# Kernel tuning notes

Measured on AMD Instinct MI355X. Metric: run time of the kernel, lower is better.

## Reference

```python
import jax, jax.numpy as jnp
import numpy as np

N = 8192        # n_nodes
F = 256         # n_features
RES_H = 512     # n_res_hidden
REP_H = 256     # n_rep_hidden
EMB = 128       # embed_dim
E = 262144      # n_edges
GAMMA = 0.1


def setup_inputs() -> dict:
    key = jax.random.key(0)
    ks = jax.random.split(key, 20)
    w = lambda k, shape, s=0.05: (jax.random.normal(k, shape, jnp.float32) * s)
    return {
        "x": jax.random.normal(ks[0], (N, F), jnp.float32),
        "edge_index": jax.random.randint(ks[1], (2, E), 0, N),
        # res_model: Linear(N,RES_H)+ReLU, Linear(RES_H,F)+ReLU
        "res_W1": w(ks[2], (N, RES_H)), "res_b1": jnp.zeros((RES_H,), jnp.float32),
        "res_W2": w(ks[3], (RES_H, F)), "res_b2": jnp.zeros((F,), jnp.float32),
        "fc_W1": w(ks[4], (F, REP_H)), "fc_b1": jnp.zeros((REP_H,), jnp.float32),
        "fc_W2": w(ks[5], (REP_H, REP_H)), "fc_b2": jnp.zeros((REP_H,), jnp.float32),
        # rep_gcn: GCNConv(F,REP_H,norm=False), GCNConv(REP_H,REP_H), GCNConv(REP_H,EMB)
        "g_W0": w(ks[6], (F, REP_H)), "g_b0": jnp.zeros((REP_H,), jnp.float32),
        "g_W1": w(ks[7], (REP_H, REP_H)), "g_b1": jnp.zeros((REP_H,), jnp.float32),
        "g_W2": w(ks[8], (REP_H, EMB)), "g_b2": jnp.zeros((EMB,), jnp.float32),
        # dec_fc: Linear(EMB,REP_H)+ReLU, Linear(REP_H,F)+ReLU
        "dec_W1": w(ks[9], (EMB, REP_H)), "dec_b1": jnp.zeros((REP_H,), jnp.float32),
        "dec_W2": w(ks[10], (REP_H, F)), "dec_b2": jnp.zeros((F,), jnp.float32),
    }


def _gcn(h, src, dst, W, b, normalize):
    """PyG GCNConv: transform then aggregate src->dst; sym-norm with self loops if normalize."""
    h = h @ W
    if normalize:
        ones = jnp.ones(src.shape[0], h.dtype)
        deg = jax.ops.segment_sum(ones, dst, num_segments=N) + 1.0  # +1 self loop
        dinv = jax.lax.rsqrt(deg)
        coef = dinv[src] * dinv[dst]
        agg = jax.ops.segment_sum(h[src] * coef[:, None], dst, num_segments=N)
        agg = agg + h * (dinv * dinv)[:, None]  # self-loop message
    else:
        agg = jax.ops.segment_sum(h[src], dst, num_segments=N)
    return agg + b


def _fwd(x, edge_index, res_W1, res_b1, res_W2, res_b2, fc_W1, fc_b1, fc_W2, fc_b2,
         g_W0, g_b0, g_W1, g_b1, g_W2, g_b2, dec_W1, dec_b1, dec_W2, dec_b2):
    relu = jax.nn.relu
    src, dst = edge_index[0], edge_index[1]
    # dense adjacency (to_dense_adj accumulates edge weights = 1)
    A = jnp.zeros((N, N), x.dtype).at[src, dst].add(1.0)
    # residual model over adjacency rows
    R = relu(relu(A @ res_W1 + res_b1) @ res_W2 + res_b2)  # [N, F]
    # GCN layer 0 (normalize=False)
    H = relu(_gcn(x, src, dst, g_W0, g_b0, False))
    # layer 1
    R_l = relu(R @ fc_W1 + fc_b1)
    H = relu(_gcn(H * jnp.exp(-GAMMA * R_l), src, dst, g_W1, g_b1, True))
    # layer 2
    R_l = relu(R_l @ fc_W2 + fc_b2)
    H = relu(_gcn(H * jnp.exp(-GAMMA * R_l), src, dst, g_W2, g_b2, True))  # [N, EMB]
    X_hat = relu(relu(H @ dec_W1 + dec_b1) @ dec_W2 + dec_b2)  # [N, F]
    A_hat = H @ H.T  # [N, N]
    return X_hat, A_hat, R


def reference(x, edge_index, res_W1, res_b1, res_W2, res_b2, fc_W1, fc_b1, fc_W2, fc_b2,
              g_W0, g_b0, g_W1, g_b1, g_W2, g_b2, dec_W1, dec_b1, dec_W2, dec_b2):
    return _fwd(x, edge_index, res_W1, res_b1, res_W2, res_b2, fc_W1, fc_b1, fc_W2, fc_b2,
                g_W0, g_b0, g_W1, g_b1, g_W2, g_b2, dec_W1, dec_b1, dec_W2, dec_b2)
```

## Files before the change

### kernel.cpp

```cpp
#include <hip/hip_runtime.h>
#include <cstddef>
#include <cstdint>

#define NN   8192
#define FF   256
#define RESH 512
#define REPH 256
#define EMBD 128
#define EE   262144
#define GAMMA_ 0.1f

typedef __attribute__((ext_vector_type(8))) short bf16x8;
typedef __attribute__((ext_vector_type(4))) float f32x4;

__device__ inline void f2hilo(float x, short& h, short& l) {
  unsigned u = __float_as_uint(x);
  unsigned r = u + 0x7FFFu + ((u >> 16) & 1u);
  h = (short)(r >> 16);
  float hf = __uint_as_float(r & 0xFFFF0000u);
  float lf = x - hf;
  unsigned u2 = __float_as_uint(lf);
  unsigned r2 = u2 + 0x7FFFu + ((u2 >> 16) & 1u);
  l = (short)(r2 >> 16);
}


__global__ void count_kernel(const int* __restrict__ ei, int* __restrict__ cnt_src,
                             int* __restrict__ cnt_dst) {
  int e = blockIdx.x * blockDim.x + threadIdx.x;
  if (e < EE) {
    atomicAdd(&cnt_src[ei[e]], 1);
    atomicAdd(&cnt_dst[ei[EE + e]], 1);
  }
}

__global__ void scan_kernel(const int* __restrict__ cnt_src, const int* __restrict__ cnt_dst,
                            int* __restrict__ off_src, int* __restrict__ off_dst) {
  const int* cnt = blockIdx.x ? cnt_dst : cnt_src;
  int* off = blockIdx.x ? off_dst : off_src;
  __shared__ int sm[1024];
  int carry = 0;
  for (int ch = 0; ch < NN / 1024; ++ch) {
    int idx = ch * 1024 + threadIdx.x;
    int v = cnt[idx];
    int x = v;
    sm[threadIdx.x] = x;
    __syncthreads();
    for (int ofs = 1; ofs < 1024; ofs <<= 1) {
      int y = (threadIdx.x >= ofs) ? sm[threadIdx.x - ofs] : 0;
      __syncthreads();
      x += y;
      sm[threadIdx.x] = x;
      __syncthreads();
    }
    off[idx] = x - v + carry;
    carry += sm[1023];
    __syncthreads();
  }
  if (threadIdx.x == 0) off[NN] = carry;
}

__global__ void fill_kernel(const int* __restrict__ ei, const int* __restrict__ off_src,
                            const int* __restrict__ off_dst, int* __restrict__ cur_src,
                            int* __restrict__ cur_dst, int* __restrict__ adj_src,
                            int* __restrict__ adj_dst) {
  int e = blockIdx.x * blockDim.x + threadIdx.x;
  if (e < EE) {
    int s = ei[e], d = ei[EE + e];
    int ps = atomicAdd(&cur_src[s], 1);
    adj_src[off_src[s] + ps] = d;
    int pd = atomicAdd(&cur_dst[d], 1);
    adj_dst[off_dst[d] + pd] = s;
  }
}

__global__ void dinv_kernel(const int* __restrict__ cnt_dst, float* __restrict__ dinv) {
  int n = blockIdx.x * blockDim.x + threadIdx.x;
  if (n < NN) dinv[n] = rsqrtf((float)cnt_dst[n] + 1.0f);
}

__global__ __launch_bounds__(256) void s1_kernel(const float* __restrict__ W1,
    const float* __restrict__ b1, const int* __restrict__ off_src,
    const int* __restrict__ adj_src, float* __restrict__ S1) {
  int i = blockIdx.x, t = threadIdx.x;
  int beg = off_src[i], end = off_src[i + 1];
  float a0 = 0.f, a1 = 0.f;
#pragma unroll 4
  for (int k = beg; k < end; ++k) {
    int d = adj_src[k];
    const float* row = W1 + (size_t)d * RESH;
    a0 += row[t];
    a1 += row[t + 256];
  }
  S1[(size_t)i * RESH + t]       = fmaxf(a0 + b1[t], 0.f);
  S1[(size_t)i * RESH + t + 256] = fmaxf(a1 + b1[t + 256], 0.f);
}

__global__ __launch_bounds__(256) void agg0_kernel(const float* __restrict__ h,
    const float* __restrict__ b, const int* __restrict__ off_dst,
    const int* __restrict__ adj_dst, float* __restrict__ out) {
  int d = blockIdx.x, t = threadIdx.x;
  int beg = off_dst[d], end = off_dst[d + 1];
  float acc = 0.f;
#pragma unroll 4
  for (int k = beg; k < end; ++k) {
    int s = adj_dst[k];
    acc += h[(size_t)s * REPH + t];
  }
  out[(size_t)d * REPH + t] = fmaxf(acc + b[t], 0.f);
}

__global__ void aggn_kernel(const float* __restrict__ h, const float* __restrict__ b,
    const float* __restrict__ dinv, const int* __restrict__ off_dst,
    const int* __restrict__ adj_dst, float* __restrict__ out, int C) {
  int d = blockIdx.x, t = threadIdx.x;
  int beg = off_dst[d], end = off_dst[d + 1];
  float acc = 0.f;
#pragma unroll 4
  for (int k = beg; k < end; ++k) {
    int s = adj_dst[k];
    acc += h[(size_t)s * C + t] * dinv[s];
  }
  float dd = dinv[d];
  float v = acc * dd + h[(size_t)d * C + t] * dd * dd + b[t];
  out[(size_t)d * C + t] = fmaxf(v, 0.f);
}

struct WDesc { const float* src; short* h; short* l; int K; int N; };
struct WTab { WDesc d[8]; };

__global__ void prep_w(WTab tab) {
  WDesc d = tab.d[blockIdx.y];
  int total = d.K * d.N;
  for (int i = blockIdx.x * 256 + threadIdx.x; i < total; i += 128 * 256) {
    int n = i / d.K, k = i - n * d.K;
    float x = d.src[(size_t)k * d.N + n];
    short hh, ll;
    f2hilo(x, hh, ll);
    d.h[i] = hh;
    d.l[i] = ll;
  }
}

__global__ void conv_h(const float* __restrict__ Hf, short* __restrict__ Hh,
                       short* __restrict__ Hl) {
  int i = blockIdx.x * 256 + threadIdx.x;
  float x = Hf[i];
  short hh, ll;
  f2hilo(x, hh, ll);
  Hh[i] = hh;
  Hl[i] = ll;
}

__global__ __launch_bounds__(256) void gemmW(const float* __restrict__ A,
    const float* __restrict__ Rm, const short* __restrict__ Wh,
    const short* __restrict__ Wl, const float* __restrict__ bias,
    float* __restrict__ C, int K, int Nc, int doRelu) {
  const int w = threadIdx.x >> 6, l = threadIdx.x & 63;
  const int lr = l & 15, lk = l >> 4;
  const int m0 = blockIdx.y * 64 + w * 16;
  const int n0 = blockIdx.x * 128;
  f32x4 acc[8] = {};
  const int nks = K >> 5;
  for (int ks = 0; ks < nks; ++ks) {
    const int k0 = (ks << 5) + (lk << 3);
    const float* ap = A + (size_t)(m0 + lr) * K + k0;
    float av[8];
    *(f32x4*)(av + 0) = *(const f32x4*)(ap + 0);
    *(f32x4*)(av + 4) = *(const f32x4*)(ap + 4);
    if (Rm) {
      const float* rp = Rm + (size_t)(m0 + lr) * K + k0;
      float rv[8];
      *(f32x4*)(rv + 0) = *(const f32x4*)(rp + 0);
      *(f32x4*)(rv + 4) = *(const f32x4*)(rp + 4);
#pragma unroll
      for (int j = 0; j < 8; ++j) av[j] *= expf(-GAMMA_ * rv[j]);
    }
    bf16x8 ah, al;
#pragma unroll
    for (int j = 0; j < 8; ++j) {
      short hh, ll;
      f2hilo(av[j], hh, ll);
      ah[j] = hh;
      al[j] = ll;
    }
#pragma unroll
    for (int cb = 0; cb < 8; ++cb) {
      size_t boff = (size_t)(n0 + (cb << 4) + lr) * K + k0;
      bf16x8 bh = *(const bf16x8*)(Wh + boff);
      bf16x8 bl = *(const bf16x8*)(Wl + boff);
      acc[cb] = __builtin_amdgcn_mfma_f32_16x16x32_bf16(ah, bh, acc[cb], 0, 0, 0);
      acc[cb] = __builtin_amdgcn_mfma_f32_16x16x32_bf16(al, bh, acc[cb], 0, 0, 0);
      acc[cb] = __builtin_amdgcn_mfma_f32_16x16x32_bf16(ah, bl, acc[cb], 0, 0, 0);
    }
  }
#pragma unroll
  for (int cb = 0; cb < 8; ++cb) {
    int col = n0 + (cb << 4) + lr;
    float bv = bias ? bias[col] : 0.f;
#pragma unroll
    for (int r = 0; r < 4; ++r) {
      int row = m0 + (lk << 2) + r;
      float v = acc[cb][r] + bv;
      if (doRelu) v = fmaxf(v, 0.f);
      C[(size_t)row * Nc + col] = v;
    }
  }
}

__global__ __launch_bounds__(256) void ahat_mfma(const short* __restrict__ Hh,
    const short* __restrict__ Hl, float* __restrict__ C) {
  const int w = threadIdx.x >> 6, l = threadIdx.x & 63;
  const int lr = l & 15, lk = l >> 4;
  const int bi = blockIdx.y * 128 + w * 32;
  const int bj = blockIdx.x * 128;
  f32x4 acc[2][8] = {};
#pragma unroll
  for (int ks = 0; ks < 4; ++ks) {
    const int k0 = (ks << 5) + (lk << 3);
    bf16x8 ah[2], al[2];
#pragma unroll
    for (int rb = 0; rb < 2; ++rb) {
      size_t off = (size_t)(bi + (rb << 4) + lr) * EMBD + k0;
      ah[rb] = *(const bf16x8*)(Hh + off);
      al[rb] = *(const bf16x8*)(Hl + off);
    }
#pragma unroll
    for (int cb = 0; cb < 8; ++cb) {
      size_t off = (size_t)(bj + (cb << 4) + lr) * EMBD + k0;
      bf16x8 bh = *(const bf16x8*)(Hh + off);
      bf16x8 bl = *(const bf16x8*)(Hl + off);
#pragma unroll
      for (int rb = 0; rb < 2; ++rb) {
        acc[rb][cb] = __builtin_amdgcn_mfma_f32_16x16x32_bf16(ah[rb], bh, acc[rb][cb], 0, 0, 0);
        acc[rb][cb] = __builtin_amdgcn_mfma_f32_16x16x32_bf16(al[rb], bh, acc[rb][cb], 0, 0, 0);
        acc[rb][cb] = __builtin_amdgcn_mfma_f32_16x16x32_bf16(ah[rb], bl, acc[rb][cb], 0, 0, 0);
      }
    }
  }
#pragma unroll
  for (int rb = 0; rb < 2; ++rb)
#pragma unroll
    for (int cb = 0; cb < 8; ++cb) {
      int row = bi + (rb << 4) + (lk << 2);
      int col = bj + (cb << 4) + lr;
#pragma unroll
      for (int r = 0; r < 4; ++r)
        C[(size_t)(row + r) * NN + col] = acc[rb][cb][r];
    }
}


extern "C" void kernel_launch(void* const* d_in, const int* in_sizes, int n_in,
                              void* d_out, int out_size, void* d_ws, size_t ws_size,
                              hipStream_t stream) {
  const float* x      = (const float*)d_in[0];
  const int*   ei     = (const int*)d_in[1];
  const float* res_W1 = (const float*)d_in[2];
  const float* res_b1 = (const float*)d_in[3];
  const float* res_W2 = (const float*)d_in[4];
  const float* res_b2 = (const float*)d_in[5];
  const float* fc_W1  = (const float*)d_in[6];
  const float* fc_b1  = (const float*)d_in[7];
  const float* fc_W2  = (const float*)d_in[8];
  const float* fc_b2  = (const float*)d_in[9];
  const float* g_W0   = (const float*)d_in[10];
  const float* g_b0   = (const float*)d_in[11];
  const float* g_W1   = (const float*)d_in[12];
  const float* g_b1   = (const float*)d_in[13];
  const float* g_W2   = (const float*)d_in[14];
  const float* g_b2   = (const float*)d_in[15];
  const float* dec_W1 = (const float*)d_in[16];
  const float* dec_b1 = (const float*)d_in[17];
  const float* dec_W2 = (const float*)d_in[18];
  const float* dec_b2 = (const float*)d_in[19];

  float* out   = (float*)d_out;
  float* X_hat = out;
  float* A_hat = out + (size_t)NN * FF;
  float* R     = A_hat + (size_t)NN * NN;

  char* ws = (char*)d_ws;
  size_t o = 0;
  auto alloc = [&](size_t bytes) -> void* {
    void* p = ws + o;
    o += (bytes + 1023) & ~(size_t)1023;
    return p;
  };
  int* cnt_src = (int*)alloc(NN * 4);
  int* cnt_dst = (int*)alloc(NN * 4);
  int* cur_src = (int*)alloc(NN * 4);
  int* cur_dst = (int*)alloc(NN * 4);
  int* off_src = (int*)alloc((NN + 1) * 4);
  int* off_dst = (int*)alloc((NN + 1) * 4);
  int* adj_src = (int*)alloc((size_t)EE * 4);
  int* adj_dst = (int*)alloc((size_t)EE * 4);
  float* dinv  = (float*)alloc(NN * 4);
  float* S1    = (float*)alloc((size_t)NN * RESH * 4);
  float* B1    = (float*)alloc((size_t)NN * REPH * 4);
  float* B2    = (float*)alloc((size_t)NN * REPH * 4);
  float* B3    = (float*)alloc((size_t)NN * REPH * 4);
  float* B4    = (float*)alloc((size_t)NN * REPH * 4);
  short* Wt_h  = (short*)alloc(524288 * 2);
  short* Wt_l  = (short*)alloc(524288 * 2);
  short* Hh    = (short*)alloc((size_t)NN * EMBD * 2);
  short* Hl    = (short*)alloc((size_t)NN * EMBD * 2);

  const int o_resW2 = 0;
  const int o_fcW1  = 131072;
  const int o_fcW2  = 196608;
  const int o_gW0   = 262144;
  const int o_gW1   = 327680;
  const int o_gW2   = 393216;
  const int o_decW1 = 425984;
  const int o_decW2 = 458752;

  hipMemsetAsync(cnt_src, 0, (size_t)NN * 4 * 4, stream);

  count_kernel<<<EE / 256, 256, 0, stream>>>(ei, cnt_src, cnt_dst);
  scan_kernel<<<2, 1024, 0, stream>>>(cnt_src, cnt_dst, off_src, off_dst);
  fill_kernel<<<EE / 256, 256, 0, stream>>>(ei, off_src, off_dst, cur_src, cur_dst,
                                            adj_src, adj_dst);
  dinv_kernel<<<NN / 256, 256, 0, stream>>>(cnt_dst, dinv);

  WTab tab;
  tab.d[0] = {res_W2, Wt_h + o_resW2, Wt_l + o_resW2, RESH, FF};
  tab.d[1] = {fc_W1,  Wt_h + o_fcW1,  Wt_l + o_fcW1,  FF,   REPH};
  tab.d[2] = {fc_W2,  Wt_h + o_fcW2,  Wt_l + o_fcW2,  REPH, REPH};
  tab.d[3] = {g_W0,   Wt_h + o_gW0,   Wt_l + o_gW0,   FF,   REPH};
  tab.d[4] = {g_W1,   Wt_h + o_gW1,   Wt_l + o_gW1,   REPH, REPH};
  tab.d[5] = {g_W2,   Wt_h + o_gW2,   Wt_l + o_gW2,   REPH, EMBD};
  tab.d[6] = {dec_W1, Wt_h + o_decW1, Wt_l + o_decW1, EMBD, REPH};
  tab.d[7] = {dec_W2, Wt_h + o_decW2, Wt_l + o_decW2, REPH, FF};
  prep_w<<<dim3(128, 8), 256, 0, stream>>>(tab);

  s1_kernel<<<NN, 256, 0, stream>>>(res_W1, res_b1, off_src, adj_src, S1);
  gemmW<<<dim3(FF / 128, NN / 64), 256, 0, stream>>>(S1, nullptr, Wt_h + o_resW2,
      Wt_l + o_resW2, res_b2, R, RESH, FF, 1);
  gemmW<<<dim3(REPH / 128, NN / 64), 256, 0, stream>>>(x, nullptr, Wt_h + o_gW0,
      Wt_l + o_gW0, nullptr, B1, FF, REPH, 0);
  agg0_kernel<<<NN, REPH, 0, stream>>>(B1, g_b0, off_dst, adj_dst, B2);
  gemmW<<<dim3(REPH / 128, NN / 64), 256, 0, stream>>>(R, nullptr, Wt_h + o_fcW1,
      Wt_l + o_fcW1, fc_b1, B3, FF, REPH, 1);
  gemmW<<<dim3(REPH / 128, NN / 64), 256, 0, stream>>>(B2, B3, Wt_h + o_gW1,
      Wt_l + o_gW1, nullptr, B1, REPH, REPH, 0);
  aggn_kernel<<<NN, REPH, 0, stream>>>(B1, g_b1, dinv, off_dst, adj_dst, B2, REPH);
  gemmW<<<dim3(REPH / 128, NN / 64), 256, 0, stream>>>(B3, nullptr, Wt_h + o_fcW2,
      Wt_l + o_fcW2, fc_b2, B4, REPH, REPH, 1);
  gemmW<<<dim3(EMBD / 128, NN / 64), 256, 0, stream>>>(B2, B4, Wt_h + o_gW2,
      Wt_l + o_gW2, nullptr, B3, REPH, EMBD, 0);
  aggn_kernel<<<NN, EMBD, 0, stream>>>(B3, g_b2, dinv, off_dst, adj_dst, B1, EMBD);
  conv_h<<<(NN * EMBD) / 256, 256, 0, stream>>>(B1, Hh, Hl);
  gemmW<<<dim3(REPH / 128, NN / 64), 256, 0, stream>>>(B1, nullptr, Wt_h + o_decW1,
      Wt_l + o_decW1, dec_b1, B2, EMBD, REPH, 1);
  gemmW<<<dim3(FF / 128, NN / 64), 256, 0, stream>>>(B2, nullptr, Wt_h + o_decW2,
      Wt_l + o_decW2, dec_b2, X_hat, REPH, FF, 1);
  ahat_mfma<<<dim3(NN / 128, NN / 128), 256, 0, stream>>>(Hh, Hl, A_hat);
}
```

Baseline: 881.3 us.

## Pre-split activations into bf16 hi/lo in producers and exploit A_hat symmetry

Result: faster. 800.2 us (-9.2%).

```diff
diff --git a/kernel.cpp b/kernel.cpp
--- a/kernel.cpp
+++ b/kernel.cpp
@@ -1,6 +1,7 @@
 #include <hip/hip_runtime.h>
 #include <cstddef>
 #include <cstdint>
+#include <math.h>
 
 #define NN   8192
 #define FF   256
@@ -12,6 +13,7 @@
 
 typedef __attribute__((ext_vector_type(8))) short bf16x8;
 typedef __attribute__((ext_vector_type(4))) float f32x4;
+typedef __attribute__((ext_vector_type(4))) short s16x4;
 
 __device__ inline void f2hilo(float x, short& h, short& l) {
   unsigned u = __float_as_uint(x);
@@ -81,7 +83,7 @@
 
 __global__ __launch_bounds__(256) void s1_kernel(const float* __restrict__ W1,
     const float* __restrict__ b1, const int* __restrict__ off_src,
-    const int* __restrict__ adj_src, float* __restrict__ S1) {
+    const int* __restrict__ adj_src, short* __restrict__ S1h, short* __restrict__ S1l) {
   int i = blockIdx.x, t = threadIdx.x;
   int beg = off_src[i], end = off_src[i + 1];
   float a0 = 0.f, a1 = 0.f;
@@ -92,13 +94,21 @@
     a0 += row[t];
     a1 += row[t + 256];
   }
-  S1[(size_t)i * RESH + t]       = fmaxf(a0 + b1[t], 0.f);
-  S1[(size_t)i * RESH + t + 256] = fmaxf(a1 + b1[t + 256], 0.f);
-}
-
-__global__ __launch_bounds__(256) void agg0_kernel(const float* __restrict__ h,
-    const float* __restrict__ b, const int* __restrict__ off_dst,
-    const int* __restrict__ adj_dst, float* __restrict__ out) {
+  float v0 = fmaxf(a0 + b1[t], 0.f);
+  float v1 = fmaxf(a1 + b1[t + 256], 0.f);
+  short hh, ll;
+  f2hilo(v0, hh, ll);
+  S1h[(size_t)i * RESH + t] = hh;
+  S1l[(size_t)i * RESH + t] = ll;
+  f2hilo(v1, hh, ll);
+  S1h[(size_t)i * RESH + t + 256] = hh;
+  S1l[(size_t)i * RESH + t + 256] = ll;
+}
+
+__global__ __launch_bounds__(256) void agg0_fused(const float* __restrict__ h,
+    const float* __restrict__ b, const float* __restrict__ mod,
+    const int* __restrict__ off_dst, const int* __restrict__ adj_dst,
+    short* __restrict__ oh, short* __restrict__ ol) {
   int d = blockIdx.x, t = threadIdx.x;
   int beg = off_dst[d], end = off_dst[d + 1];
   float acc = 0.f;
@@ -107,12 +117,18 @@
     int s = adj_dst[k];
     acc += h[(size_t)s * REPH + t];
   }
-  out[(size_t)d * REPH + t] = fmaxf(acc + b[t], 0.f);
-}
-
-__global__ void aggn_kernel(const float* __restrict__ h, const float* __restrict__ b,
-    const float* __restrict__ dinv, const int* __restrict__ off_dst,
-    const int* __restrict__ adj_dst, float* __restrict__ out, int C) {
+  size_t o = (size_t)d * REPH + t;
+  float v = fmaxf(acc + b[t], 0.f) * expf(-GAMMA_ * mod[o]);
+  short hh, ll;
+  f2hilo(v, hh, ll);
+  oh[o] = hh;
+  ol[o] = ll;
+}
+
+__global__ void aggn_fused(const float* __restrict__ h, const float* __restrict__ b,
+    const float* __restrict__ dinv, const float* __restrict__ mod,
+    const int* __restrict__ off_dst, const int* __restrict__ adj_dst,
+    short* __restrict__ oh, short* __restrict__ ol, int C) {
   int d = blockIdx.x, t = threadIdx.x;
   int beg = off_dst[d], end = off_dst[d + 1];
   float acc = 0.f;
@@ -122,8 +138,13 @@
     acc += h[(size_t)s * C + t] * dinv[s];
   }
   float dd = dinv[d];
-  float v = acc * dd + h[(size_t)d * C + t] * dd * dd + b[t];
-  out[(size_t)d * C + t] = fmaxf(v, 0.f);
+  size_t o = (size_t)d * C + t;
+  float v = fmaxf(acc * dd + h[o] * dd * dd + b[t], 0.f);
+  if (mod) v *= expf(-GAMMA_ * mod[o]);
+  short hh, ll;
+  f2hilo(v, hh, ll);
+  oh[o] = hh;
+  ol[o] = ll;
 }
 
 struct WDesc { const float* src; short* h; short* l; int K; int N; };
@@ -142,50 +163,41 @@
   }
 }
 
-__global__ void conv_h(const float* __restrict__ Hf, short* __restrict__ Hh,
-                       short* __restrict__ Hl) {
-  int i = blockIdx.x * 256 + threadIdx.x;
-  float x = Hf[i];
-  short hh, ll;
-  f2hilo(x, hh, ll);
-  Hh[i] = hh;
-  Hl[i] = ll;
-}
-
-__global__ __launch_bounds__(256) void gemmW(const float* __restrict__ A,
-    const float* __restrict__ Rm, const short* __restrict__ Wh,
-    const short* __restrict__ Wl, const float* __restrict__ bias,
-    float* __restrict__ C, int K, int Nc, int doRelu) {
+__global__ void conv_split(const float* __restrict__ in, short* __restrict__ oh,
+                           short* __restrict__ ol) {
+  int i = (blockIdx.x * 256 + threadIdx.x) * 4;
+  f32x4 v = *(const f32x4*)(in + i);
+  s16x4 vh, vl;
+#pragma unroll
+  for (int j = 0; j < 4; ++j) {
+    short hh, ll;
+    f2hilo(v[j], hh, ll);
+    vh[j] = hh;
+    vl[j] = ll;
+  }
+  *(s16x4*)(oh + i) = vh;
+  *(s16x4*)(ol + i) = vl;
+}
+
+template<int CB>
+__global__ __launch_bounds__(256) void gemmS(const short* __restrict__ Ah,
+    const short* __restrict__ Al, const short* __restrict__ Wh,
+    const short* __restrict__ Wl, const float* __restrict__ bias, int doRelu,
+    float* __restrict__ outF, short* __restrict__ outH, short* __restrict__ outL,
+    int K, int Nc) {
   const int w = threadIdx.x >> 6, l = threadIdx.x & 63;
   const int lr = l & 15, lk = l >> 4;
   const int m0 = blockIdx.y * 64 + w * 16;
-  const int n0 = blockIdx.x * 128;
-  f32x4 acc[8] = {};
+  const int n0 = blockIdx.x * (CB * 16);
+  f32x4 acc[CB] = {};
   const int nks = K >> 5;
   for (int ks = 0; ks < nks; ++ks) {
     const int k0 = (ks << 5) + (lk << 3);
-    const float* ap = A + (size_t)(m0 + lr) * K + k0;
-    float av[8];
-    *(f32x4*)(av + 0) = *(const f32x4*)(ap + 0);
-    *(f32x4*)(av + 4) = *(const f32x4*)(ap + 4);
-    if (Rm) {
-      const float* rp = Rm + (size_t)(m0 + lr) * K + k0;
-      float rv[8];
-      *(f32x4*)(rv + 0) = *(const f32x4*)(rp + 0);
-      *(f32x4*)(rv + 4) = *(const f32x4*)(rp + 4);
-#pragma unroll
-      for (int j = 0; j < 8; ++j) av[j] *= expf(-GAMMA_ * rv[j]);
-    }
-    bf16x8 ah, al;
-#pragma unroll
-    for (int j = 0; j < 8; ++j) {
-      short hh, ll;
-      f2hilo(av[j], hh, ll);
-      ah[j] = hh;
-      al[j] = ll;
-    }
-#pragma unroll
-    for (int cb = 0; cb < 8; ++cb) {
+    size_t aoff = (size_t)(m0 + lr) * K + k0;
+    bf16x8 ah = *(const bf16x8*)(Ah + aoff);
+    bf16x8 al = *(const bf16x8*)(Al + aoff);
+#pragma unroll
+    for (int cb = 0; cb < CB; ++cb) {
       size_t boff = (size_t)(n0 + (cb << 4) + lr) * K + k0;
       bf16x8 bh = *(const bf16x8*)(Wh + boff);
       bf16x8 bl = *(const bf16x8*)(Wl + boff);
@@ -195,7 +207,7 @@
     }
   }
 #pragma unroll
-  for (int cb = 0; cb < 8; ++cb) {
+  for (int cb = 0; cb < CB; ++cb) {
     int col = n0 + (cb << 4) + lr;
     float bv = bias ? bias[col] : 0.f;
 #pragma unroll
@@ -203,17 +215,31 @@
       int row = m0 + (lk << 2) + r;
       float v = acc[cb][r] + bv;
       if (doRelu) v = fmaxf(v, 0.f);
-      C[(size_t)row * Nc + col] = v;
-    }
-  }
-}
-
-__global__ __launch_bounds__(256) void ahat_mfma(const short* __restrict__ Hh,
+      size_t off = (size_t)row * Nc + col;
+      if (outF) outF[off] = v;
+      if (outH) {
+        short hh, ll;
+        f2hilo(v, hh, ll);
+        outH[off] = hh;
+        outL[off] = ll;
+      }
+    }
+  }
+}
+
+__global__ __launch_bounds__(256) void ahat_sym(const short* __restrict__ Hh,
     const short* __restrict__ Hl, float* __restrict__ C) {
+  __shared__ float sm[128][129];
+  int z = blockIdx.x;
+  int b = (int)((sqrtf(8.f * (float)z + 1.f) - 1.f) * 0.5f);
+  while ((b + 1) * (b + 2) / 2 <= z) ++b;
+  while (b * (b + 1) / 2 > z) --b;
+  int a = z - b * (b + 1) / 2;
+  const int bi = a * 128, bj = b * 128;
+  const bool mirror = (a != b);
   const int w = threadIdx.x >> 6, l = threadIdx.x & 63;
   const int lr = l & 15, lk = l >> 4;
-  const int bi = blockIdx.y * 128 + w * 32;
-  const int bj = blockIdx.x * 128;
+  const int ri = w * 32;
   f32x4 acc[2][8] = {};
 #pragma unroll
   for (int ks = 0; ks < 4; ++ks) {
@@ -221,7 +247,7 @@
     bf16x8 ah[2], al[2];
 #pragma unroll
     for (int rb = 0; rb < 2; ++rb) {
-      size_t off = (size_t)(bi + (rb << 4) + lr) * EMBD + k0;
+      size_t off = (size_t)(bi + ri + (rb << 4) + lr) * EMBD + k0;
       ah[rb] = *(const bf16x8*)(Hh + off);
       al[rb] = *(const bf16x8*)(Hl + off);
     }
@@ -242,12 +268,22 @@
   for (int rb = 0; rb < 2; ++rb)
 #pragma unroll
     for (int cb = 0; cb < 8; ++cb) {
-      int row = bi + (rb << 4) + (lk << 2);
-      int col = bj + (cb << 4) + lr;
-#pragma unroll
-      for (int r = 0; r < 4; ++r)
-        C[(size_t)(row + r) * NN + col] = acc[rb][cb][r];
-    }
+      int r0 = ri + (rb << 4) + (lk << 2);
+      int c0 = (cb << 4) + lr;
+#pragma unroll
+      for (int r = 0; r < 4; ++r) {
+        float v = acc[rb][cb][r];
+        C[(size_t)(bi + r0 + r) * NN + bj + c0] = v;
+        if (mirror) sm[r0 + r][c0] = v;
+      }
+    }
+  if (mirror) {
+    __syncthreads();
+    for (int idx = threadIdx.x; idx < 128 * 128; idx += 256) {
+      int jr = idx >> 7, c = idx & 127;
+      C[(size_t)(bj + jr) * NN + bi + c] = sm[c][jr];
+    }
+  }
 }
 
 
@@ -296,15 +332,27 @@
   int* adj_src = (int*)alloc((size_t)EE * 4);
   int* adj_dst = (int*)alloc((size_t)EE * 4);
   float* dinv  = (float*)alloc(NN * 4);
-  float* S1    = (float*)alloc((size_t)NN * RESH * 4);
-  float* B1    = (float*)alloc((size_t)NN * REPH * 4);
-  float* B2    = (float*)alloc((size_t)NN * REPH * 4);
-  float* B3    = (float*)alloc((size_t)NN * REPH * 4);
-  float* B4    = (float*)alloc((size_t)NN * REPH * 4);
   short* Wt_h  = (short*)alloc(524288 * 2);
   short* Wt_l  = (short*)alloc(524288 * 2);
-  short* Hh    = (short*)alloc((size_t)NN * EMBD * 2);
-  short* Hl    = (short*)alloc((size_t)NN * EMBD * 2);
+  const size_t SLAB = (size_t)8 * 1024 * 1024;
+  char* slabA = (char*)alloc(SLAB);
+  char* slabB = (char*)alloc(SLAB);
+  char* slabC = (char*)alloc(SLAB);
+  char* slabD = (char*)alloc(SLAB);
+  short* S1h = (short*)slabA;
+  short* Xh  = (short*)slabA;            short* Xl  = (short*)(slabA + SLAB / 2);
+  short* M1h = (short*)slabA;            short* M1l = (short*)(slabA + SLAB / 2);
+  short* M2h = (short*)slabA;            short* M2l = (short*)(slabA + SLAB / 2);
+  short* D1h = (short*)slabA;            short* D1l = (short*)(slabA + SLAB / 2);
+  short* S1l = (short*)slabB;
+  float* B3f = (float*)slabB;
+  float* B4f = (float*)slabB;
+  float* G2f = (float*)slabB;
+  short* Rh  = (short*)slabC;            short* Rl  = (short*)(slabC + SLAB / 2);
+  float* B1f = (float*)slabC;
+  float* G1f = (float*)slabC;
+  short* B3h = (short*)slabD;            short* B3l = (short*)(slabD + SLAB / 2);
+  short* Hh  = (short*)slabD;            short* Hl  = (short*)(slabD + (size_t)2 * 1024 * 1024);
 
   const int o_resW2 = 0;
   const int o_fcW1  = 131072;
@@ -334,26 +382,28 @@
   tab.d[7] = {dec_W2, Wt_h + o_decW2, Wt_l + o_decW2, REPH, FF};
   prep_w<<<dim3(128, 8), 256, 0, stream>>>(tab);
 
-  s1_kernel<<<NN, 256, 0, stream>>>(res_W1, res_b1, off_src, adj_src, S1);
-  gemmW<<<dim3(FF / 128, NN / 64), 256, 0, stream>>>(S1, nullptr, Wt_h + o_resW2,
-      Wt_l + o_resW2, res_b2, R, RESH, FF, 1);
-  gemmW<<<dim3(REPH / 128, NN / 64), 256, 0, stream>>>(x, nullptr, Wt_h + o_gW0,
-      Wt_l + o_gW0, nullptr, B1, FF, REPH, 0);
-  agg0_kernel<<<NN, REPH, 0, stream>>>(B1, g_b0, off_dst, adj_dst, B2);
-  gemmW<<<dim3(REPH / 128, NN / 64), 256, 0, stream>>>(R, nullptr, Wt_h + o_fcW1,
-      Wt_l + o_fcW1, fc_b1, B3, FF, REPH, 1);
-  gemmW<<<dim3(REPH / 128, NN / 64), 256, 0, stream>>>(B2, B3, Wt_h + o_gW1,
-      Wt_l + o_gW1, nullptr, B1, REPH, REPH, 0);
-  aggn_kernel<<<NN, REPH, 0, stream>>>(B1, g_b1, dinv, off_dst, adj_dst, B2, REPH);
-  gemmW<<<dim3(REPH / 128, NN / 64), 256, 0, stream>>>(B3, nullptr, Wt_h + o_fcW2,
-      Wt_l + o_fcW2, fc_b2, B4, REPH, REPH, 1);
-  gemmW<<<dim3(EMBD / 128, NN / 64), 256, 0, stream>>>(B2, B4, Wt_h + o_gW2,
-      Wt_l + o_gW2, nullptr, B3, REPH, EMBD, 0);
-  aggn_kernel<<<NN, EMBD, 0, stream>>>(B3, g_b2, dinv, off_dst, adj_dst, B1, EMBD);
-  conv_h<<<(NN * EMBD) / 256, 256, 0, stream>>>(B1, Hh, Hl);
-  gemmW<<<dim3(REPH / 128, NN / 64), 256, 0, stream>>>(B1, nullptr, Wt_h + o_decW1,
-      Wt_l + o_decW1, dec_b1, B2, EMBD, REPH, 1);
-  gemmW<<<dim3(FF / 128, NN / 64), 256, 0, stream>>>(B2, nullptr, Wt_h + o_decW2,
-      Wt_l + o_decW2, dec_b2, X_hat, REPH, FF, 1);
-  ahat_mfma<<<dim3(NN / 128, NN / 128), 256, 0, stream>>>(Hh, Hl, A_hat);
-}
+  s1_kernel<<<NN, 256, 0, stream>>>(res_W1, res_b1, off_src, adj_src, S1h, S1l);
+  gemmS<8><<<dim3(2, 128), 256, 0, stream>>>(S1h, S1l, Wt_h + o_resW2, Wt_l + o_resW2,
+      res_b2, 1, R, Rh, Rl, RESH, FF);
+  gemmS<8><<<dim3(2, 128), 256, 0, stream>>>(Rh, Rl, Wt_h + o_fcW1, Wt_l + o_fcW1,
+      fc_b1, 1, B3f, B3h, B3l, FF, REPH);
+  conv_split<<<(NN * FF) / 1024, 256, 0, stream>>>(x, Xh, Xl);
+  gemmS<8><<<dim3(2, 128), 256, 0, stream>>>(Xh, Xl, Wt_h + o_gW0, Wt_l + o_gW0,
+      nullptr, 0, B1f, nullptr, nullptr, FF, REPH);
+  agg0_fused<<<NN, REPH, 0, stream>>>(B1f, g_b0, B3f, off_dst, adj_dst, M1h, M1l);
+  gemmS<8><<<dim3(2, 128), 256, 0, stream>>>(M1h, M1l, Wt_h + o_gW1, Wt_l + o_gW1,
+      nullptr, 0, G1f, nullptr, nullptr, REPH, REPH);
+  gemmS<8><<<dim3(2, 128), 256, 0, stream>>>(B3h, B3l, Wt_h + o_fcW2, Wt_l + o_fcW2,
+      fc_b2, 1, B4f, nullptr, nullptr, REPH, REPH);
+  aggn_fused<<<NN, REPH, 0, stream>>>(G1f, g_b1, dinv, B4f, off_dst, adj_dst,
+                                      M2h, M2l, REPH);
+  gemmS<4><<<dim3(2, 128), 256, 0, stream>>>(M2h, M2l, Wt_h + o_gW2, Wt_l + o_gW2,
+      nullptr, 0, G2f, nullptr, nullptr, REPH, EMBD);
+  aggn_fused<<<NN, EMBD, 0, stream>>>(G2f, g_b2, dinv, nullptr, off_dst, adj_dst,
+                                      Hh, Hl, EMBD);
+  gemmS<8><<<dim3(2, 128), 256, 0, stream>>>(Hh, Hl, Wt_h + o_decW1, Wt_l + o_decW1,
+      dec_b1, 1, nullptr, D1h, D1l, EMBD, REPH);
+  gemmS<8><<<dim3(2, 128), 256, 0, stream>>>(D1h, D1l, Wt_h + o_decW2, Wt_l + o_decW2,
+      dec_b2, 1, X_hat, nullptr, nullptr, REPH, FF);
+  ahat_sym<<<2080, 256, 0, stream>>>(Hh, Hl, A_hat);
+}
```
